# Performance work log

Hardware: AMD Instinct MI355X
Metric: run time of the kernel (lower is better)

## Reference

```python
import jax, jax.numpy as jnp
import numpy as np

H = 64
VOCAB = 64
READ_FREQ = 16


def setup_inputs() -> dict:
    key = jax.random.key(0)
    ks = jax.random.split(key, 16)
    B, L, M = 512, 2048, 256
    seq = jax.random.randint(ks[0], (B, L), 0, VOCAB)
    memory = jax.random.normal(ks[1], (B, M, H), dtype=jnp.float32)
    s = 0.1
    return {
        "seq": seq,
        "memory": memory,
        "embed_w": jax.random.normal(ks[2], (VOCAB, H), jnp.float32) * s,
        "gru_w_ih": jax.random.normal(ks[3], (3 * H, 2 * H), jnp.float32) * s,
        "gru_w_hh": jax.random.normal(ks[4], (3 * H, H), jnp.float32) * s,
        "gru_b_ih": jax.random.normal(ks[5], (3 * H,), jnp.float32) * s,
        "gru_b_hh": jax.random.normal(ks[6], (3 * H,), jnp.float32) * s,
        "key_w": jax.random.normal(ks[7], (H, H), jnp.float32) * s,
        "key_b": jax.random.normal(ks[8], (H,), jnp.float32) * s,
        "val_w": jax.random.normal(ks[9], (H, H), jnp.float32) * s,
        "val_b": jax.random.normal(ks[10], (H,), jnp.float32) * s,
        "query_w": jax.random.normal(ks[11], (H, H), jnp.float32) * s,
        "query_b": jax.random.normal(ks[12], (H,), jnp.float32) * s,
        "head_w": jax.random.normal(ks[13], (VOCAB, H), jnp.float32) * s,
        "head_b": jax.random.normal(ks[14], (VOCAB,), jnp.float32) * s,
    }


def _forward(seq, memory, embed_w, gru_w_ih, gru_w_hh, gru_b_ih, gru_b_hh,
             key_w, key_b, val_w, val_b, query_w, query_b, head_w, head_b):
    B, L = seq.shape
    scale = 1.0 / (H ** 0.5)
    # memory is fixed: precompute keys/values once (B, M, H)
    k = jnp.einsum("bmh,kh->bmk", memory, key_w) + key_b
    v = jnp.einsum("bmh,kh->bmk", memory, val_w) + val_b
    # embed all tokens up front: (B, L, H) -> chunks (C, F, B, H)
    emb = embed_w[seq]
    C = L // READ_FREQ
    emb_chunks = emb.reshape(B, C, READ_FREQ, H).transpose(1, 2, 0, 3)

    def gru_step(carry, x_t):
        h, retrieved = carry
        inp = jnp.concatenate([x_t, retrieved], axis=-1)  # (B, 2H)
        gi = inp @ gru_w_ih.T + gru_b_ih                   # (B, 3H)
        gh = h @ gru_w_hh.T + gru_b_hh                     # (B, 3H)
        i_r, i_z, i_n = jnp.split(gi, 3, axis=-1)
        h_r, h_z, h_n = jnp.split(gh, 3, axis=-1)
        r = jax.nn.sigmoid(i_r + h_r)
        z = jax.nn.sigmoid(i_z + h_z)
        n = jnp.tanh(i_n + r * h_n)
        h_new = (1.0 - z) * n + z * h
        return (h_new, retrieved), None

    def chunk_step(h, chunk_emb):  # chunk_emb: (READ_FREQ, B, H)
        q = h @ query_w.T + query_b                        # (B, H)
        scores = jnp.einsum("bh,bmh->bm", q, k) * scale
        w = jax.nn.softmax(scores, axis=-1)
        retrieved = jnp.einsum("bm,bmh->bh", w, v)
        (h, _), _ = jax.lax.scan(gru_step, (h, retrieved), chunk_emb)
        return h, None

    h0 = jnp.zeros((B, H), dtype=memory.dtype)
    h, _ = jax.lax.scan(chunk_step, h0, emb_chunks)
    return h @ head_w.T + head_b                            # (B, VOCAB)


def reference(seq, memory, embed_w, gru_w_ih, gru_w_hh, gru_b_ih, gru_b_hh,
              key_w, key_b, val_w, val_b, query_w, query_b, head_w, head_b):
    return _forward(seq, memory, embed_w, gru_w_ih, gru_w_hh, gru_b_ih, gru_b_hh,
                    key_w, key_b, val_w, val_b, query_w, query_b, head_w, head_b)
```

## Files before the change

### kernel.cpp

```cpp
#include <hip/hip_runtime.h>
#include <hip/hip_fp16.h>


#define B_ 512
#define L_ 2048
#define M_ 256
#define H_ 64
#define C_ 128
#define F_ 16

typedef float v2f __attribute__((ext_vector_type(2)));
typedef _Float16 h2v __attribute__((ext_vector_type(2)));

#if __has_builtin(__builtin_amdgcn_fdot2)
__device__ __forceinline__ float FDOT2(h2v a, h2v b, float c) {
    return __builtin_amdgcn_fdot2(a, b, c, false);
}
#else
__device__ __forceinline__ float FDOT2(h2v a, h2v b, float c) {
    return c + (float)a[0]*(float)b[0] + (float)a[1]*(float)b[1];
}
#endif

__device__ __forceinline__ h2v bch(unsigned u) { return __builtin_bit_cast(h2v, u); }
__device__ __forceinline__ unsigned rl_u(unsigned v, int lane) {
    return (unsigned)__builtin_amdgcn_readlane((int)v, lane);
}
__device__ __forceinline__ float rl(float v, int lane) {
    return __int_as_float(__builtin_amdgcn_readlane(__float_as_int(v), lane));
}
__device__ __forceinline__ unsigned pkrtz(float a, float b) {
    auto r = __builtin_amdgcn_cvt_pkrtz(a, b);
    return __builtin_bit_cast(unsigned, r);
}
__device__ __forceinline__ float dot4(float4 a, float4 b) {
    return a.x*b.x + a.y*b.y + a.z*b.z + a.w*b.w;
}
__device__ __forceinline__ float fast_rcp(float x) { return __builtin_amdgcn_rcpf(x); }
__device__ __forceinline__ float sigm(float x) { return fast_rcp(1.f + __expf(-x)); }
__device__ __forceinline__ float tanh_f(float x) {
    float e2 = __expf(-2.f * fabsf(x));
    return copysignf((1.f - e2) * fast_rcp(1.f + e2), x);
}
__device__ __forceinline__ unsigned h2rn(float a, float b) {
    __half2 h = __floats2half2_rn(a, b);
    return __builtin_bit_cast(unsigned, h);
}

#define WS_KT    0u
#define WS_V     16777216u
#define WS_G4    33554432u
#define WS_WPHH  33619968u
#define WS_WR    33644544u
#define WS_KQP   33669120u
#define WS_VWP   33685504u
#define WS_KQF   33701888u
#define WS_BQ    33718272u
#define WS_KQV   33718528u
#define WS_C0    33718784u
#define WS_CB    33719040u

#define S_V    0u
#define S_P    33792u
#define SMEM_BYTES 34304u

__global__ void pack_weights(const float* __restrict__ w_ih,
                             const float* __restrict__ w_hh,
                             const float* __restrict__ vw,
                             unsigned* __restrict__ WPhh2,
                             unsigned* __restrict__ WR2p,
                             float4* __restrict__ VWP)
{
    int idx = blockIdx.x * 256 + threadIdx.x;
    if (idx < 6144) {
        int j = idx & 63, t = idx >> 6, g = t % 3, k2 = t / 3;
        const float* s = w_hh + (g*64 + j)*64 + 2*k2;
        WPhh2[idx] = h2rn(s[0], s[1]);
    } else if (idx < 12288) {
        int i = idx - 6144;
        int j = i & 63, t = i >> 6, g = t % 3, k2 = t / 3;
        const float* s = w_ih + (g*64 + j)*128 + 64 + 2*k2;
        WR2p[i] = h2rn(s[0], s[1]);
    } else if (idx < 13312) {
        int i = idx - 12288;
        int j = i & 63, k4 = i >> 6;
        const float* s = vw + j*64 + 4*k4;
        VWP[i] = make_float4(s[0], s[1], s[2], s[3]);
    }
}

__global__ __launch_bounds__(64) void fold_kq(const float* __restrict__ kw,
                                              const float* __restrict__ qw,
                                              const float* __restrict__ kb,
                                              const float* __restrict__ qb,
                                              float* __restrict__ KQf,
                                              float* __restrict__ bqv,
                                              float* __restrict__ kqv,
                                              float* __restrict__ c0p)
{
    int d = blockIdx.x, j = threadIdx.x;
    __shared__ float kcol[64], kbs[64], qbs[64];
    kcol[j] = kw[j*64 + d];
    kbs[j]  = kb[j];
    qbs[j]  = qb[j];
    __syncthreads();
    float acc = 0.f, accq = 0.f;
    for (int t = 0; t < 64; ++t) {
        float kc = kcol[t];
        acc  += kc * qw[t*64 + j];
        accq += kc * qbs[t];
    }
    KQf[d*64 + j] = acc;
    if (j == 0) kqv[d] = accq;
    if (d == 0) {
        float vb = 0.f;
        for (int t = 0; t < 64; ++t) vb += kbs[t] * qw[t*64 + j];
        bqv[j] = vb;
        if (j == 0) {
            float c0 = 0.f;
            for (int t = 0; t < 64; ++t) c0 += kbs[t] * qbs[t];
            *c0p = c0;
        }
    }
}

__global__ __launch_bounds__(256) void pack_kq(const float* __restrict__ KQf,
                                               float4* __restrict__ KQP)
{
    int i = blockIdx.x * 256 + threadIdx.x;
    if (i < 1024) {
        int o = i & 63, k4 = i >> 6;
        KQP[i] = make_float4(KQf[(4*k4+0)*64 + o], KQf[(4*k4+1)*64 + o],
                             KQf[(4*k4+2)*64 + o], KQf[(4*k4+3)*64 + o]);
    }
}

__global__ __launch_bounds__(64) void build_G(const float* __restrict__ embed_w,
                                              const float* __restrict__ w_ih,
                                              const float* __restrict__ b_ih,
                                              float4* __restrict__ G4)
{
    int v = blockIdx.x, j = threadIdx.x;
    __shared__ float e_s[64];
    e_s[j] = embed_w[v*64 + j];
    __syncthreads();
    float a0 = b_ih[j], a1 = b_ih[64 + j], a2 = b_ih[128 + j];
    for (int k = 0; k < 64; ++k) {
        float e = e_s[k];
        a0 += e * w_ih[j*128 + k];
        a1 += e * w_ih[(64 + j)*128 + k];
        a2 += e * w_ih[(128 + j)*128 + k];
    }
    G4[v*64 + j] = make_float4(a0, a1, a2, 0.f);
}

__global__ __launch_bounds__(256) void compute_kv(const float* __restrict__ memory,
                                                  const float* __restrict__ bqv,
                                                  const float* __restrict__ val_b,
                                                  const float4* __restrict__ KQP,
                                                  const float4* __restrict__ VWP,
                                                  const float* __restrict__ kqv,
                                                  const float* __restrict__ c0p,
                                                  unsigned* __restrict__ kT2,
                                                  unsigned* __restrict__ vT2,
                                                  float* __restrict__ cB)
{
    int wid = threadIdx.x >> 6;
    int o   = threadIdx.x & 63;
    int row = blockIdx.x * 4 + wid;
    int b = row >> 8, m = row & 255;
    __shared__ __align__(16) float mem_s[4][64];
    __shared__ float avs[4][64];
    mem_s[wid][o] = memory[(size_t)row * 64 + o];
    __syncthreads();
    float ak = bqv[o], av = val_b[o], ac = *c0p;
    const float4* m4  = (const float4*)mem_s[wid];
    const float4* kq4 = (const float4*)kqv;
#pragma unroll
    for (int k4 = 0; k4 < 16; ++k4) {
        float4 mm = m4[k4];
        ak += dot4(mm, KQP[k4*64 + o]);
        av += dot4(mm, VWP[k4*64 + o]);
        ac += dot4(mm, kq4[k4]);
    }
    float nb = __shfl_xor(ak, 1);
    if ((o & 1) == 0)
        kT2[((size_t)b*32 + (o >> 1))*256 + m] = h2rn(ak, nb);
    avs[wid][o] = av;
    if (o == 0) cB[row] = ac;
    __syncthreads();
    if ((wid & 1) == 0) {
        vT2[((size_t)b*64 + o)*128 + (m >> 1)] = h2rn(avs[wid][o], avs[wid+1][o]);
    }
}

#define GRU_STEP(cg0, cg1, cg2) do {                                        \
    float gr = RrB, gz = RzB, gn = bhn;                                     \
    _Pragma("unroll")                                                       \
    for (int kp = 0; kp < 32; ++kp) {                                       \
        h2v hhp = bch(rl_u(hpu, 2*kp));                                     \
        gr = FDOT2(hhp, wr2[kp], gr);                                       \
        gz = FDOT2(hhp, wz2[kp], gz);                                       \
        gn = FDOT2(hhp, wn2[kp], gn);                                       \
    }                                                                       \
    float r_ = sigm(gr + (cg0));                                            \
    float z_ = sigm(gz + (cg1));                                            \
    float n_ = tanh_f(((cg2) + Rn) + r_ * gn);                              \
    h = fmaf(z_, h - n_, n_);                                               \
    float hx_ = __shfl_xor(h, 1);                                           \
    hpu = pkrtz(h, hx_);                                                    \
} while (0)

__global__ __launch_bounds__(64, 1) void recurrent_main(
    const int*   __restrict__ seq,
    const float* __restrict__ b_hh,
    const float* __restrict__ head_w,
    const float* __restrict__ head_b,
    const unsigned* __restrict__ kT2g,
    const unsigned* __restrict__ vT2g,
    const float4* __restrict__ G4,
    const unsigned* __restrict__ WPhh2,
    const unsigned* __restrict__ WR2p,
    const float* __restrict__ cB,
    float* __restrict__ out)
{
    const int b = blockIdx.x;
    const int j = threadIdx.x;

    extern __shared__ __align__(16) char smem[];

    {
        const uint4* vg4 = (const uint4*)(vT2g + (size_t)b * 8192);
        uint4* vls4 = (uint4*)(smem + S_V);
#pragma unroll
        for (int i = 0; i < 32; ++i) {
            int t = i*64 + j;
            vls4[(t >> 5)*33 + (t & 31)] = vg4[t];
        }
    }

    uint4 kk[32];
    {
        const uint4* kTg = (const uint4*)(kT2g + (size_t)b * 8192);
#pragma unroll
        for (int t = 0; t < 32; ++t) kk[t] = kTg[t*64 + j];
    }

    h2v wr2[32], wz2[32], wn2[32];
#pragma unroll
    for (int k2 = 0; k2 < 32; ++k2) {
        wr2[k2] = bch(WPhh2[(k2*3 + 0)*64 + j]);
        wz2[k2] = bch(WPhh2[(k2*3 + 1)*64 + j]);
        wn2[k2] = bch(WPhh2[(k2*3 + 2)*64 + j]);
    }
    h2v rr2[32], rz2[32], rn2[32];
#pragma unroll
    for (int k2 = 0; k2 < 32; ++k2) {
        rr2[k2] = bch(WR2p[(k2*3 + 0)*64 + j]);
        rz2[k2] = bch(WR2p[(k2*3 + 1)*64 + j]);
        rn2[k2] = bch(WR2p[(k2*3 + 2)*64 + j]);
    }

    float h = 0.f;
    unsigned hpu = 0u;
    const float bhr = b_hh[j], bhz = b_hh[64 + j], bhn = b_hh[128 + j];
    const float4 cc = *(const float4*)(cB + (size_t)b*256 + 4*j);

    const int* seqb = seq + (size_t)b * L_;
    const uint4* vrow = (const uint4*)(smem + S_V) + j*33;
    const uint4* p4   = (const uint4*)(smem + S_P);
    __builtin_amdgcn_wave_barrier();

    for (int c = 0; c < C_; ++c) {
        const int c16 = c * F_;

        const int4 pA = *(const int4*)(seqb + c16);
        const int4 pB = *(const int4*)(seqb + c16 + 4);
        const int4 pC = *(const int4*)(seqb + c16 + 8);
        const int4 pD = *(const int4*)(seqb + c16 + 12);

        float s0 = cc.x, s1 = cc.y, s2 = cc.z, s3 = cc.w;
#pragma unroll
        for (int t = 0; t < 32; ++t) {
            h2v qq = bch(rl_u(hpu, 2*t));
            s0 = FDOT2(bch(kk[t].x), qq, s0);
            s1 = FDOT2(bch(kk[t].y), qq, s1);
            s2 = FDOT2(bch(kk[t].z), qq, s2);
            s3 = FDOT2(bch(kk[t].w), qq, s3);
        }
        const float scale = 0.125f;
        float4 p;
        p.x = __expf(s0*scale); p.y = __expf(s1*scale);
        p.z = __expf(s2*scale); p.w = __expf(s3*scale);
        float sum = (p.x + p.y) + (p.z + p.w);
#pragma unroll
        for (int o = 32; o > 0; o >>= 1) sum += __shfl_xor(sum, o);
        float inv = fast_rcp(sum);
        *(uint2*)(smem + S_P + (size_t)j*8) =
            make_uint2(pkrtz(p.x, p.y), pkrtz(p.z, p.w));
        __builtin_amdgcn_wave_barrier();

        float r0 = 0.f, r1 = 0.f, r2 = 0.f, r3 = 0.f;
#pragma unroll 8
        for (int qd = 0; qd < 32; ++qd) {
            uint4 vv = vrow[qd];
            uint4 pp = p4[qd];
            r0 = FDOT2(bch(pp.x), bch(vv.x), r0);
            r1 = FDOT2(bch(pp.y), bch(vv.y), r1);
            r2 = FDOT2(bch(pp.z), bch(vv.z), r2);
            r3 = FDOT2(bch(pp.w), bch(vv.w), r3);
        }
        float ret = ((r0 + r1) + (r2 + r3)) * inv;

        float rx = __shfl_xor(ret, 1);
        unsigned rpu = pkrtz(ret, rx);
        float Rr = 0.f, Rz = 0.f, Rn = 0.f;
#pragma unroll
        for (int k2 = 0; k2 < 32; ++k2) {
            h2v rr = bch(rl_u(rpu, 2*k2));
            Rr = FDOT2(rr, rr2[k2], Rr);
            Rz = FDOT2(rr, rz2[k2], Rz);
            Rn = FDOT2(rr, rn2[k2], Rn);
        }
        const float RrB = Rr + bhr, RzB = Rz + bhz;

#pragma unroll 1
        for (int g = 0; g < 4; ++g) {
            const bool gb1 = (g & 1), gb2 = (g & 2);
            int4 tlo, thi, tg;
            tlo.x = gb1 ? pB.x : pA.x; tlo.y = gb1 ? pB.y : pA.y;
            tlo.z = gb1 ? pB.z : pA.z; tlo.w = gb1 ? pB.w : pA.w;
            thi.x = gb1 ? pD.x : pC.x; thi.y = gb1 ? pD.y : pC.y;
            thi.z = gb1 ? pD.z : pC.z; thi.w = gb1 ? pD.w : pC.w;
            tg.x = gb2 ? thi.x : tlo.x; tg.y = gb2 ? thi.y : tlo.y;
            tg.z = gb2 ? thi.z : tlo.z; tg.w = gb2 ? thi.w : tlo.w;
            const float4 gA = G4[tg.x*64 + j];
            const float4 gB = G4[tg.y*64 + j];
            const float4 gC = G4[tg.z*64 + j];
            const float4 gD = G4[tg.w*64 + j];

            GRU_STEP(gA.x, gA.y, gA.z);
            GRU_STEP(gB.x, gB.y, gB.z);
            GRU_STEP(gC.x, gC.y, gC.z);
            GRU_STEP(gD.x, gD.y, gD.z);
        }
    }

    float o = head_b[j];
#pragma unroll
    for (int k4 = 0; k4 < 16; ++k4) {
        float h0 = rl(h, 4*k4+0), h1 = rl(h, 4*k4+1);
        float h2 = rl(h, 4*k4+2), h3 = rl(h, 4*k4+3);
        const float* hw = head_w + j*64 + 4*k4;
        o += h0*hw[0] + h1*hw[1] + h2*hw[2] + h3*hw[3];
    }
    out[(size_t)b*64 + j] = o;
}

extern "C" void kernel_launch(void* const* d_in, const int* in_sizes, int n_in,
                              void* d_out, int out_size, void* d_ws, size_t ws_size,
                              hipStream_t stream) {
    const int*   seq      = (const int*)  d_in[0];
    const float* memory   = (const float*)d_in[1];
    const float* embed_w  = (const float*)d_in[2];
    const float* w_ih     = (const float*)d_in[3];
    const float* w_hh     = (const float*)d_in[4];
    const float* b_ih     = (const float*)d_in[5];
    const float* b_hh     = (const float*)d_in[6];
    const float* key_w    = (const float*)d_in[7];
    const float* key_b    = (const float*)d_in[8];
    const float* val_w    = (const float*)d_in[9];
    const float* val_b    = (const float*)d_in[10];
    const float* query_w  = (const float*)d_in[11];
    const float* query_b  = (const float*)d_in[12];
    const float* head_w   = (const float*)d_in[13];
    const float* head_b   = (const float*)d_in[14];

    char* ws = (char*)d_ws;
    unsigned* kT2  = (unsigned*)(ws + WS_KT);
    unsigned* vT2  = (unsigned*)(ws + WS_V);
    float4*   G4   = (float4*)  (ws + WS_G4);
    unsigned* WPhh2 = (unsigned*)(ws + WS_WPHH);
    unsigned* WR2p  = (unsigned*)(ws + WS_WR);
    float4*   KQP   = (float4*)  (ws + WS_KQP);
    float4*   VWP   = (float4*)  (ws + WS_VWP);
    float*    KQf   = (float*)   (ws + WS_KQF);
    float*    bqv   = (float*)   (ws + WS_BQ);
    float*    kqv   = (float*)   (ws + WS_KQV);
    float*    c0p   = (float*)   (ws + WS_C0);
    float*    cB    = (float*)   (ws + WS_CB);

    (void)hipFuncSetAttribute((const void*)recurrent_main,
                              hipFuncAttributeMaxDynamicSharedMemorySize,
                              (int)SMEM_BYTES);

    pack_weights<<<64, 256, 0, stream>>>(w_ih, w_hh, val_w, WPhh2, WR2p, VWP);
    fold_kq<<<64, 64, 0, stream>>>(key_w, query_w, key_b, query_b,
                                   KQf, bqv, kqv, c0p);
    pack_kq<<<4, 256, 0, stream>>>(KQf, KQP);
    build_G<<<64, 64, 0, stream>>>(embed_w, w_ih, b_ih, G4);
    compute_kv<<<(B_*M_)/4, 256, 0, stream>>>(memory, bqv, val_b, KQP, VWP,
                                              kqv, c0p, kT2, vT2, cB);
    recurrent_main<<<B_, 64, SMEM_BYTES, stream>>>(seq, b_hh, head_w, head_b,
                                                   kT2, vT2, G4, WPhh2, WR2p, cB,
                                                   (float*)d_out);
}
```

Measured before the change: 1.446 ms.

## Move attention keys to LDS, pass softmax weights via lane shuffles, scalarize token indices

Keys are no longer held in 128 VGPRs per lane. They are staged into LDS and streamed from there on every chunk, which frees registers at the cost of extra LDS reads. The softmax probabilities are no longer written to LDS behind a wave barrier; each lane reads them from other lanes with readlane broadcasts. Token indices are made wave-uniform with readfirstlane, so the per-step selects run on scalar registers. LDS usage roughly doubles per block.

```diff
diff --git a/kernel.cpp b/kernel.cpp
--- a/kernel.cpp
+++ b/kernel.cpp
@@ -60,9 +60,9 @@
 #define WS_C0    33718784u
 #define WS_CB    33719040u
 
-#define S_V    0u
-#define S_P    33792u
-#define SMEM_BYTES 34304u
+#define S_KT   0u
+#define S_V    32768u
+#define SMEM_BYTES 66560u
 
 __global__ void pack_weights(const float* __restrict__ w_ih,
                              const float* __restrict__ w_hh,
@@ -228,8 +228,13 @@
     const int j = threadIdx.x;
 
     extern __shared__ __align__(16) char smem[];
+    const uint4* kT2_lds = (const uint4*)(smem + S_KT);
 
     {
+        const uint4* kTg = (const uint4*)(kT2g + (size_t)b * 8192);
+        uint4* kTls = (uint4*)(smem + S_KT);
+#pragma unroll
+        for (int i = 0; i < 32; ++i) kTls[i*64 + j] = kTg[i*64 + j];
         const uint4* vg4 = (const uint4*)(vT2g + (size_t)b * 8192);
         uint4* vls4 = (uint4*)(smem + S_V);
 #pragma unroll
@@ -237,13 +242,6 @@
             int t = i*64 + j;
             vls4[(t >> 5)*33 + (t & 31)] = vg4[t];
         }
-    }
-
-    uint4 kk[32];
-    {
-        const uint4* kTg = (const uint4*)(kT2g + (size_t)b * 8192);
-#pragma unroll
-        for (int t = 0; t < 32; ++t) kk[t] = kTg[t*64 + j];
     }
 
     h2v wr2[32], wz2[32], wn2[32];
@@ -268,47 +266,65 @@
 
     const int* seqb = seq + (size_t)b * L_;
     const uint4* vrow = (const uint4*)(smem + S_V) + j*33;
-    const uint4* p4   = (const uint4*)(smem + S_P);
     __builtin_amdgcn_wave_barrier();
 
     for (int c = 0; c < C_; ++c) {
         const int c16 = c * F_;
 
-        const int4 pA = *(const int4*)(seqb + c16);
-        const int4 pB = *(const int4*)(seqb + c16 + 4);
-        const int4 pC = *(const int4*)(seqb + c16 + 8);
-        const int4 pD = *(const int4*)(seqb + c16 + 12);
+        const int4 qA = *(const int4*)(seqb + c16);
+        const int4 qB = *(const int4*)(seqb + c16 + 4);
+        const int4 qC = *(const int4*)(seqb + c16 + 8);
+        const int4 qD = *(const int4*)(seqb + c16 + 12);
+        const int tA0 = __builtin_amdgcn_readfirstlane(qA.x);
+        const int tA1 = __builtin_amdgcn_readfirstlane(qA.y);
+        const int tA2 = __builtin_amdgcn_readfirstlane(qA.z);
+        const int tA3 = __builtin_amdgcn_readfirstlane(qA.w);
+        const int tB0 = __builtin_amdgcn_readfirstlane(qB.x);
+        const int tB1 = __builtin_amdgcn_readfirstlane(qB.y);
+        const int tB2 = __builtin_amdgcn_readfirstlane(qB.z);
+        const int tB3 = __builtin_amdgcn_readfirstlane(qB.w);
+        const int tC0 = __builtin_amdgcn_readfirstlane(qC.x);
+        const int tC1 = __builtin_amdgcn_readfirstlane(qC.y);
+        const int tC2 = __builtin_amdgcn_readfirstlane(qC.z);
+        const int tC3 = __builtin_amdgcn_readfirstlane(qC.w);
+        const int tD0 = __builtin_amdgcn_readfirstlane(qD.x);
+        const int tD1 = __builtin_amdgcn_readfirstlane(qD.y);
+        const int tD2 = __builtin_amdgcn_readfirstlane(qD.z);
+        const int tD3 = __builtin_amdgcn_readfirstlane(qD.w);
 
         float s0 = cc.x, s1 = cc.y, s2 = cc.z, s3 = cc.w;
-#pragma unroll
+#pragma unroll 8
         for (int t = 0; t < 32; ++t) {
             h2v qq = bch(rl_u(hpu, 2*t));
-            s0 = FDOT2(bch(kk[t].x), qq, s0);
-            s1 = FDOT2(bch(kk[t].y), qq, s1);
-            s2 = FDOT2(bch(kk[t].z), qq, s2);
-            s3 = FDOT2(bch(kk[t].w), qq, s3);
+            uint4 kk = kT2_lds[t*64 + j];
+            s0 = FDOT2(bch(kk.x), qq, s0);
+            s1 = FDOT2(bch(kk.y), qq, s1);
+            s2 = FDOT2(bch(kk.z), qq, s2);
+            s3 = FDOT2(bch(kk.w), qq, s3);
         }
         const float scale = 0.125f;
         float4 p;
         p.x = __expf(s0*scale); p.y = __expf(s1*scale);
         p.z = __expf(s2*scale); p.w = __expf(s3*scale);
+        const unsigned ppu0 = pkrtz(p.x, p.y);
+        const unsigned ppu1 = pkrtz(p.z, p.w);
         float sum = (p.x + p.y) + (p.z + p.w);
 #pragma unroll
         for (int o = 32; o > 0; o >>= 1) sum += __shfl_xor(sum, o);
         float inv = fast_rcp(sum);
-        *(uint2*)(smem + S_P + (size_t)j*8) =
-            make_uint2(pkrtz(p.x, p.y), pkrtz(p.z, p.w));
-        __builtin_amdgcn_wave_barrier();
 
         float r0 = 0.f, r1 = 0.f, r2 = 0.f, r3 = 0.f;
 #pragma unroll 8
         for (int qd = 0; qd < 32; ++qd) {
             uint4 vv = vrow[qd];
-            uint4 pp = p4[qd];
-            r0 = FDOT2(bch(pp.x), bch(vv.x), r0);
-            r1 = FDOT2(bch(pp.y), bch(vv.y), r1);
-            r2 = FDOT2(bch(pp.z), bch(vv.z), r2);
-            r3 = FDOT2(bch(pp.w), bch(vv.w), r3);
+            unsigned px = rl_u(ppu0, 2*qd);
+            unsigned py = rl_u(ppu1, 2*qd);
+            unsigned pz = rl_u(ppu0, 2*qd + 1);
+            unsigned pw = rl_u(ppu1, 2*qd + 1);
+            r0 = FDOT2(bch(px), bch(vv.x), r0);
+            r1 = FDOT2(bch(py), bch(vv.y), r1);
+            r2 = FDOT2(bch(pz), bch(vv.z), r2);
+            r3 = FDOT2(bch(pw), bch(vv.w), r3);
         }
         float ret = ((r0 + r1) + (r2 + r3)) * inv;
 
@@ -327,17 +343,14 @@
 #pragma unroll 1
         for (int g = 0; g < 4; ++g) {
             const bool gb1 = (g & 1), gb2 = (g & 2);
-            int4 tlo, thi, tg;
-            tlo.x = gb1 ? pB.x : pA.x; tlo.y = gb1 ? pB.y : pA.y;
-            tlo.z = gb1 ? pB.z : pA.z; tlo.w = gb1 ? pB.w : pA.w;
-            thi.x = gb1 ? pD.x : pC.x; thi.y = gb1 ? pD.y : pC.y;
-            thi.z = gb1 ? pD.z : pC.z; thi.w = gb1 ? pD.w : pC.w;
-            tg.x = gb2 ? thi.x : tlo.x; tg.y = gb2 ? thi.y : tlo.y;
-            tg.z = gb2 ? thi.z : tlo.z; tg.w = gb2 ? thi.w : tlo.w;
-            const float4 gA = G4[tg.x*64 + j];
-            const float4 gB = G4[tg.y*64 + j];
-            const float4 gC = G4[tg.z*64 + j];
-            const float4 gD = G4[tg.w*64 + j];
+            const int t0 = gb2 ? (gb1 ? tD0 : tC0) : (gb1 ? tB0 : tA0);
+            const int t1 = gb2 ? (gb1 ? tD1 : tC1) : (gb1 ? tB1 : tA1);
+            const int t2 = gb2 ? (gb1 ? tD2 : tC2) : (gb1 ? tB2 : tA2);
+            const int t3 = gb2 ? (gb1 ? tD3 : tC3) : (gb1 ? tB3 : tA3);
+            const float4 gA = G4[t0*64 + j];
+            const float4 gB = G4[t1*64 + j];
+            const float4 gC = G4[t2*64 + j];
+            const float4 gD = G4[t3*64 + j];
 
             GRU_STEP(gA.x, gA.y, gA.z);
             GRU_STEP(gB.x, gB.y, gB.z);
```

Measured after the change: 1.268 ms, median of 2. 1.14x faster.
